# Kernel tuning notes

Measured on AMD Instinct MI355X. Metric: run time of the kernel, lower is better.

## Reference

```python
import jax, jax.numpy as jnp
import numpy as np
from jax import lax

TAU = 0.5       # opt.tau
EPSILON = 1e-3  # opt.epsilon


def setup_inputs() -> dict:
    key = jax.random.key(0)
    k1, k2, k3, k4 = jax.random.split(key, 4)
    B, Cin, H, W = 32, 64, 64, 64
    Cout, KS = 256, 5
    x = jax.random.normal(k1, (B, Cin, H, W), dtype=jnp.float32)
    # W_ff: OIHW conv kernel (Kaiming-ish scale)
    W_ff = jax.random.normal(k2, (Cout, Cin, KS, KS), dtype=jnp.float32) * (1.0 / np.sqrt(Cin * KS * KS))
    # W_rec: 1x1 recurrent conv, stored as [out, out]; small so the LCA loop converges
    W_rec = jax.random.normal(k3, (Cout, Cout), dtype=jnp.float32) * 0.01
    threshold = 0.1 * jax.random.normal(k4, (Cout,), dtype=jnp.float32)
    return {"x": x, "W_ff": W_ff, "W_rec": W_rec, "threshold": threshold, "max_n_iter": 20}


def _fro(v):
    return jnp.linalg.norm(v.ravel())


def _forward(x, W_ff, W_rec, threshold, max_n_iter):
    max_iter = max_n_iter * int(1.0 / TAU)
    # u_0 = W_ff * input  (valid conv, no bias)  -> [B, Cout, Ho, Wo]
    u0 = lax.conv_general_dilated(x, W_ff, window_strides=(1, 1), padding='VALID',
                                  dimension_numbers=('NCHW', 'OIHW', 'NCHW'))
    thr = threshold[None, :, None, None]
    a0 = jax.nn.relu(u0 - thr)
    u_init = jnp.zeros_like(u0)

    def cond(state):
        _, _, i, converged = state
        return jnp.logical_and(jnp.logical_not(converged), i <= max_iter)

    def body(state):
        u, a, i, _ = state
        # 1x1 recurrent conv == channel matmul
        rec = jnp.einsum('oi,bixy->boxy', W_rec, a)
        u_new = (1.0 - TAU) * u + TAU * (u0 - rec)
        a_new = jax.nn.relu(u_new - thr)
        converged = (_fro(u_new - u) / _fro(u_new)) < EPSILON
        return (u_new, a_new, i + 1, converged)

    _, a_final, _, _ = lax.while_loop(cond, body, (u_init, a0, jnp.int32(0), jnp.array(False)))
    # original torch code detaches activities throughout the loop and at return
    return lax.stop_gradient(a_final)


def reference(x, W_ff, W_rec, threshold, max_n_iter):
    return _forward(x, W_ff, W_rec, threshold, max_n_iter)
```

## Files before the change

kernel.cpp:

```cpp
#include <hip/hip_runtime.h>


typedef __attribute__((ext_vector_type(8))) short short8;
typedef __attribute__((ext_vector_type(4))) float f32x4;

#define NTOT 115200
#define CHW  262144
#define HW2  4096
#define LDA  264
#define LDC  40

__device__ __forceinline__ unsigned short f2bf(float f) {
  unsigned int u = __float_as_uint(f);
  unsigned int r = u + 0x7FFFu + ((u >> 16) & 1u);
  return (unsigned short)(r >> 16);
}
__device__ __forceinline__ float bf2f(unsigned short h) {
  return __uint_as_float(((unsigned int)h) << 16);
}
__device__ __forceinline__ unsigned short f2h(float f) {
  _Float16 x = (_Float16)f;
  unsigned short r;
  __builtin_memcpy(&r, &x, 2);
  return r;
}
__device__ __forceinline__ float h2f(unsigned short h) {
  _Float16 x;
  __builtin_memcpy(&x, &h, 2);
  return (float)x;
}

__global__ void cast_weights(const float* __restrict__ wff_f,
                             const float* __restrict__ wrec_f,
                             unsigned short* __restrict__ wff,
                             unsigned short* __restrict__ wrec_sw) {
  int tid = blockIdx.x * 256 + threadIdx.x;
  if (tid < 409600) {
    int o = tid / 1600, k = tid % 1600;
    int kk = k >> 6, ci = k & 63;
    wff[tid] = f2bf(wff_f[o * 1600 + ci * 25 + kk]);
  } else if (tid < 409600 + 65536) {
    int i = tid - 409600;
    int o = i >> 8, ic = i & 255;
    wrec_sw[(((ic >> 3) << 8) + o) * 8 + (ic & 7)] = f2bf(wrec_f[i]);
  }
}

__global__ __launch_bounds__(256) void transpose_x(
    const float* __restrict__ x, unsigned short* __restrict__ xt) {
  int g = blockIdx.x * 256 + threadIdx.x;
  const float* src = x + (long)(g >> 12) * CHW + (g & 4095);
  unsigned short* dst = xt + (long)g * 64;
#pragma unroll
  for (int oct = 0; oct < 8; ++oct) {
    alignas(16) unsigned short tmp[8];
#pragma unroll
    for (int d = 0; d < 8; ++d)
      tmp[d] = f2bf(src[(oct * 8 + d) * HW2]);
    *(int4*)(dst + oct * 8) = *(const int4*)tmp;
  }
}

__global__ __launch_bounds__(256) void conv_kernel(
    const unsigned short* __restrict__ xt,
    const unsigned short* __restrict__ wff,
    unsigned short* __restrict__ u0_fl) {
  __shared__ short As[128 * LDC];
  __shared__ short Bs[128 * LDC];
  const int t = threadIdx.x;
  const int n0 = blockIdx.x * 128;
  const int oc0 = blockIdx.y * 128;
  const int lane = t & 63, w = t >> 6;
  const int q = lane >> 4, r = lane & 15;
  const int woc = w >> 1, wn = w & 1;
  const int qt = t & 3, mrow = t >> 2;

  int xbase[2];
#pragma unroll
  for (int p = 0; p < 2; ++p) {
    int n = n0 + p * 64 + mrow;
    int bb = n / 3600, rem = n - bb * 3600;
    int yy = rem / 60, xx = rem - yy * 60;
    xbase[p] = (bb * 4096 + yy * 64 + xx) * 64 + qt * 8;
  }

  f32x4 acc[4][4];
#pragma unroll
  for (int i = 0; i < 4; i++)
#pragma unroll
    for (int j = 0; j < 4; j++) acc[i][j] = (f32x4){0.f, 0.f, 0.f, 0.f};

  for (int c = 0; c < 50; ++c) {
    const int k0 = c * 32;
    const int kk = c >> 1;
    const int ky = kk / 5, kx = kk - ky * 5;
    const int choff = (ky * 64 + kx) * 64 + (c & 1) * 32;

    __syncthreads();
#pragma unroll
    for (int p = 0; p < 2; ++p) {
      int m = p * 64 + mrow;
      *(int4*)(&Bs[m * LDC + qt * 8]) =
          *(const int4*)(wff + (oc0 + m) * 1600 + k0 + qt * 8);
    }
#pragma unroll
    for (int p = 0; p < 2; ++p) {
      int m = p * 64 + mrow;
      *(int4*)(&As[m * LDC + qt * 8]) = *(const int4*)(xt + xbase[p] + choff);
    }
    __syncthreads();

    short8 xf[4], wf[4];
#pragma unroll
    for (int j = 0; j < 4; j++)
      xf[j] = *(const short8*)(&As[(wn * 64 + j * 16 + r) * LDC + q * 8]);
#pragma unroll
    for (int i = 0; i < 4; i++)
      wf[i] = *(const short8*)(&Bs[(woc * 64 + i * 16 + r) * LDC + q * 8]);
#pragma unroll
    for (int i = 0; i < 4; i++)
#pragma unroll
      for (int j = 0; j < 4; j++)
        acc[i][j] = __builtin_amdgcn_mfma_f32_16x16x32_bf16(wf[i], xf[j],
                                                            acc[i][j], 0, 0, 0);
  }

  const int tile = blockIdx.x * 2 + wn;
#pragma unroll
  for (int j = 0; j < 4; j++) {
#pragma unroll
    for (int p = 0; p < 2; p++) {
      const int w_fl = blockIdx.y * 4 + woc * 2 + p;
      alignas(16) unsigned short up[8];
#pragma unroll
      for (int d = 0; d < 4; ++d) up[d] = f2h(acc[2 * p][j][d]);
#pragma unroll
      for (int d = 0; d < 4; ++d) up[4 + d] = f2h(acc[2 * p + 1][j][d]);
      *(int4*)(&u0_fl[tile * 16384 + j * 4096 + (w_fl * 64 + q * 16 + r) * 8]) =
          *(const int4*)up;
    }
  }
}

__device__ __forceinline__ void gemm_acc8(const short* a_lds,
                                          const unsigned short* __restrict__
                                              wrec_sw,
                                          int w, int q, int r,
                                          f32x4 acc[2][4]) {
#pragma unroll
  for (int i = 0; i < 2; i++)
#pragma unroll
    for (int j = 0; j < 4; j++) acc[i][j] = (f32x4){0.f, 0.f, 0.f, 0.f};

#pragma unroll
  for (int c = 0; c < 8; ++c) {
    short8 afr[2], bfr[4];
#pragma unroll
    for (int i = 0; i < 2; i++)
      afr[i] = *(const short8*)(wrec_sw +
               (((c * 4 + q) << 8) + w * 32 + i * 16 + r) * 8);
#pragma unroll
    for (int j = 0; j < 4; j++)
      bfr[j] = *(const short8*)(&a_lds[(j * 16 + r) * LDA + c * 32 + q * 8]);
#pragma unroll
    for (int i = 0; i < 2; i++)
#pragma unroll
      for (int j = 0; j < 4; j++)
        acc[i][j] = __builtin_amdgcn_mfma_f32_16x16x32_bf16(afr[i], bfr[j],
                                                            acc[i][j], 0, 0, 0);
  }
}

template <int FIRST>
__global__ __launch_bounds__(512, 4) void iter_quad(
    const unsigned short* __restrict__ wrec_sw,
    const unsigned short* __restrict__ u0, const float* __restrict__ thr,
    const unsigned short* __restrict__ uin,
    unsigned short* __restrict__ o1, unsigned short* __restrict__ o2,
    unsigned short* __restrict__ o3, unsigned short* __restrict__ o4,
    float* __restrict__ norms, int* __restrict__ flag, int it1) {
  __shared__ short a_lds[64 * LDA];
  __shared__ float red[64];

  const int t = threadIdx.x;
  if (!FIRST) {
    if (*(volatile int*)flag) return;
    bool hit = false;
#pragma unroll
    for (int rr = 0; rr < 4; ++rr) {
      float d = 0.f, n = 0.f;
#pragma unroll
      for (int s = 0; s < 8; ++s) {
        d += norms[(it1 - 4 + rr) * 16 + s];
        n += norms[(it1 - 4 + rr) * 16 + 8 + s];
      }
      hit = hit || (d < 1e-6f * n);
    }
    if (hit) {
      if (t == 0) *flag = 1;
      return;
    }
  }

  const int lane = t & 63, w = t >> 6;
  const int q = lane >> 4, r = lane & 15;
  const unsigned base = blockIdx.x * 16384 + t * 8;

  float thc[2][4];
#pragma unroll
  for (int i = 0; i < 2; ++i) {
    float4 th = *(const float4*)(thr + w * 32 + i * 16 + q * 4);
    thc[i][0] = th.x; thc[i][1] = th.y; thc[i][2] = th.z; thc[i][3] = th.w;
  }

  int4 sv[4], u0c[4];
#pragma unroll
  for (int j = 0; j < 4; ++j) {
    u0c[j] = *(const int4*)(u0 + base + j * 4096);
    sv[j] = FIRST ? u0c[j] : *(const int4*)(uin + base + j * 4096);
  }

  float d2[4], n2[4];
#pragma unroll
  for (int p = 0; p < 4; ++p) { d2[p] = 0.f; n2[p] = 0.f; }

#define QPHASE(PH, OUT)                                                       \
  {                                                                           \
    _Pragma("unroll")                                                         \
    for (int j = 0; j < 4; ++j) {                                             \
      const unsigned short* hs = (const unsigned short*)&sv[j];               \
      _Pragma("unroll")                                                       \
      for (int i = 0; i < 2; ++i) {                                           \
        alignas(8) unsigned short ap[4];                                      \
        _Pragma("unroll")                                                     \
        for (int d = 0; d < 4; ++d) {                                         \
          float a = h2f(hs[i * 4 + d]) - thc[i][d];                           \
          ap[d] = f2bf(a > 0.f ? a : 0.f);                                    \
        }                                                                     \
        *(uint2*)(&a_lds[(j * 16 + r) * LDA + w * 32 + i * 16 + q * 4]) =     \
            *(const uint2*)ap;                                                \
      }                                                                       \
    }                                                                         \
    __syncthreads();                                                          \
    f32x4 acc[2][4];                                                          \
    gemm_acc8(a_lds, wrec_sw, w, q, r, acc);                                  \
    _Pragma("unroll")                                                         \
    for (int j = 0; j < 4; ++j) {                                             \
      const unsigned short* us = (const unsigned short*)&u0c[j];              \
      const unsigned short* hs = (const unsigned short*)&sv[j];               \
      alignas(16) unsigned short up[8];                                       \
      _Pragma("unroll")                                                       \
      for (int i = 0; i < 2; ++i)                                             \
        _Pragma("unroll")                                                     \
        for (int d = 0; d < 4; ++d) {                                         \
          float uo = (FIRST && (PH) == 1) ? 0.f : h2f(hs[i * 4 + d]);         \
          float un = 0.5f * uo + 0.5f * (h2f(us[i * 4 + d]) - acc[i][j][d]);  \
          float df = un - uo;                                                 \
          d2[(PH)-1] += df * df;                                              \
          n2[(PH)-1] += un * un;                                              \
          up[i * 4 + d] = f2h(un);                                            \
        }                                                                     \
      sv[j] = *(const int4*)up;                                               \
      *(int4*)((OUT) + base + j * 4096) = sv[j];                              \
    }                                                                         \
    __syncthreads();                                                          \
  }

  QPHASE(1, o1)
  QPHASE(2, o2)
  QPHASE(3, o3)
  QPHASE(4, o4)
#undef QPHASE

#pragma unroll
  for (int off = 32; off; off >>= 1)
#pragma unroll
    for (int p = 0; p < 4; ++p) {
      d2[p] += __shfl_down(d2[p], off, 64);
      n2[p] += __shfl_down(n2[p], off, 64);
    }
  if (lane == 0)
#pragma unroll
    for (int p = 0; p < 4; ++p) {
      red[p * 16 + w] = d2[p];
      red[p * 16 + 8 + w] = n2[p];
    }
  __syncthreads();
  if (t == 0) {
    const int slot = blockIdx.x & 7;
#pragma unroll
    for (int p = 0; p < 4; ++p) {
      float a0 = 0.f, a1 = 0.f;
#pragma unroll
      for (int s = 0; s < 8; ++s) {
        a0 += red[p * 16 + s];
        a1 += red[p * 16 + 8 + s];
      }
      atomicAdd(&norms[(it1 + p) * 16 + slot], a0);
      atomicAdd(&norms[(it1 + p) * 16 + 8 + slot], a1);
    }
  }
}

template <int FIRST>
__global__ __launch_bounds__(512, 4) void iter_pair(
    const unsigned short* __restrict__ wrec_sw,
    const unsigned short* __restrict__ u0, const float* __restrict__ thr,
    const unsigned short* __restrict__ uin,
    unsigned short* __restrict__ uA, unsigned short* __restrict__ uB,
    float* __restrict__ norms, int* __restrict__ flag, int itA) {
  __shared__ short a_lds[64 * LDA];
  __shared__ float red[32];

  const int t = threadIdx.x;
  if (!FIRST) {
    if (*(volatile int*)flag) return;
    float dA = 0.f, nA = 0.f, dB = 0.f, nB = 0.f;
#pragma unroll
    for (int s = 0; s < 8; ++s) {
      dA += norms[(itA - 2) * 16 + s];
      nA += norms[(itA - 2) * 16 + 8 + s];
      dB += norms[(itA - 1) * 16 + s];
      nB += norms[(itA - 1) * 16 + 8 + s];
    }
    if (dA < 1e-6f * nA || dB < 1e-6f * nB) {
      if (t == 0) *flag = 1;
      return;
    }
  }

  const int lane = t & 63, w = t >> 6;
  const int q = lane >> 4, r = lane & 15;
  const unsigned base = blockIdx.x * 16384 + t * 8;

  float thc[2][4];
#pragma unroll
  for (int i = 0; i < 2; ++i) {
    float4 th = *(const float4*)(thr + w * 32 + i * 16 + q * 4);
    thc[i][0] = th.x; thc[i][1] = th.y; thc[i][2] = th.z; thc[i][3] = th.w;
  }

  int4 sv[4], u0c[4];
#pragma unroll
  for (int j = 0; j < 4; ++j) {
    u0c[j] = *(const int4*)(u0 + base + j * 4096);
    sv[j] = FIRST ? u0c[j] : *(const int4*)(uin + base + j * 4096);
  }

#pragma unroll
  for (int j = 0; j < 4; ++j) {
    const unsigned short* hs = (const unsigned short*)&sv[j];
#pragma unroll
    for (int i = 0; i < 2; ++i) {
      alignas(8) unsigned short ap[4];
#pragma unroll
      for (int d = 0; d < 4; ++d) {
        float a = h2f(hs[i * 4 + d]) - thc[i][d];
        ap[d] = f2bf(a > 0.f ? a : 0.f);
      }
      *(uint2*)(&a_lds[(j * 16 + r) * LDA + w * 32 + i * 16 + q * 4]) =
          *(const uint2*)ap;
    }
  }
  __syncthreads();

  f32x4 acc[2][4];
  gemm_acc8(a_lds, wrec_sw, w, q, r, acc);

  float d2A = 0.f, n2A = 0.f;
#pragma unroll
  for (int j = 0; j < 4; ++j) {
    const unsigned short* us = (const unsigned short*)&u0c[j];
    const unsigned short* hs = (const unsigned short*)&sv[j];
    alignas(16) unsigned short up[8];
#pragma unroll
    for (int i = 0; i < 2; ++i)
#pragma unroll
      for (int d = 0; d < 4; ++d) {
        float uo = FIRST ? 0.f : h2f(hs[i * 4 + d]);
        float un = 0.5f * uo + 0.5f * (h2f(us[i * 4 + d]) - acc[i][j][d]);
        float df = un - uo;
        d2A += df * df;
        n2A += un * un;
        up[i * 4 + d] = f2h(un);
      }
    sv[j] = *(const int4*)up;
    *(int4*)(uA + base + j * 4096) = sv[j];
  }
  __syncthreads();

#pragma unroll
  for (int j = 0; j < 4; ++j) {
    const unsigned short* hs = (const unsigned short*)&sv[j];
#pragma unroll
    for (int i = 0; i < 2; ++i) {
      alignas(8) unsigned short ap[4];
#pragma unroll
      for (int d = 0; d < 4; ++d) {
        float a = h2f(hs[i * 4 + d]) - thc[i][d];
        ap[d] = f2bf(a > 0.f ? a : 0.f);
      }
      *(uint2*)(&a_lds[(j * 16 + r) * LDA + w * 32 + i * 16 + q * 4]) =
          *(const uint2*)ap;
    }
  }
  __syncthreads();

  gemm_acc8(a_lds, wrec_sw, w, q, r, acc);

  float d2B = 0.f, n2B = 0.f;
#pragma unroll
  for (int j = 0; j < 4; ++j) {
    const unsigned short* us = (const unsigned short*)&u0c[j];
    const unsigned short* hs = (const unsigned short*)&sv[j];
    alignas(16) unsigned short up[8];
#pragma unroll
    for (int i = 0; i < 2; ++i)
#pragma unroll
      for (int d = 0; d < 4; ++d) {
        float uo = h2f(hs[i * 4 + d]);
        float un = 0.5f * uo + 0.5f * (h2f(us[i * 4 + d]) - acc[i][j][d]);
        float df = un - uo;
        d2B += df * df;
        n2B += un * un;
        up[i * 4 + d] = f2h(un);
      }
    *(int4*)(uB + base + j * 4096) = *(const int4*)up;
  }

#pragma unroll
  for (int off = 32; off; off >>= 1) {
    d2A += __shfl_down(d2A, off, 64);
    n2A += __shfl_down(n2A, off, 64);
    d2B += __shfl_down(d2B, off, 64);
    n2B += __shfl_down(n2B, off, 64);
  }
  if (lane == 0) {
    red[w] = d2A; red[8 + w] = n2A; red[16 + w] = d2B; red[24 + w] = n2B;
  }
  __syncthreads();
  if (t == 0) {
    float a0 = 0.f, a1 = 0.f, a2 = 0.f, a3 = 0.f;
#pragma unroll
    for (int s = 0; s < 8; ++s) {
      a0 += red[s]; a1 += red[8 + s]; a2 += red[16 + s]; a3 += red[24 + s];
    }
    const int slot = blockIdx.x & 7;
    atomicAdd(&norms[itA * 16 + slot], a0);
    atomicAdd(&norms[itA * 16 + 8 + slot], a1);
    atomicAdd(&norms[(itA + 1) * 16 + slot], a2);
    atomicAdd(&norms[(itA + 1) * 16 + 8 + slot], a3);
  }
}

template <int FIRST, int ROWS>
__global__ __launch_bounds__(512, 4) void iter_one(
    const unsigned short* __restrict__ wrec_sw,
    const unsigned short* __restrict__ u0, const float* __restrict__ thr,
    const unsigned short* __restrict__ uin, unsigned short* __restrict__ uout,
    float* __restrict__ norms, int* __restrict__ flag, int it) {
  __shared__ short a_lds[64 * LDA];
  __shared__ float red[16];

  const int t = threadIdx.x;
  if (!FIRST) {
    if (*(volatile int*)flag) return;
    bool hit = false;
#pragma unroll
    for (int rr = 0; rr < ROWS; ++rr) {
      float d = 0.f, n = 0.f;
#pragma unroll
      for (int s = 0; s < 8; ++s) {
        d += norms[(it - ROWS + rr) * 16 + s];
        n += norms[(it - ROWS + rr) * 16 + 8 + s];
      }
      hit = hit || (d < 1e-6f * n);
    }
    if (hit) {
      if (t == 0) *flag = 1;
      return;
    }
  }

  const int lane = t & 63, w = t >> 6;
  const int q = lane >> 4, r = lane & 15;
  const unsigned base = blockIdx.x * 16384 + t * 8;

  float thc[2][4];
#pragma unroll
  for (int i = 0; i < 2; ++i) {
    float4 th = *(const float4*)(thr + w * 32 + i * 16 + q * 4);
    thc[i][0] = th.x; thc[i][1] = th.y; thc[i][2] = th.z; thc[i][3] = th.w;
  }

  int4 sv[4], u0c[4];
#pragma unroll
  for (int j = 0; j < 4; ++j) {
    u0c[j] = *(const int4*)(u0 + base + j * 4096);
    sv[j] = FIRST ? u0c[j] : *(const int4*)(uin + base + j * 4096);
  }

#pragma unroll
  for (int j = 0; j < 4; ++j) {
    const unsigned short* hs = (const unsigned short*)&sv[j];
#pragma unroll
    for (int i = 0; i < 2; ++i) {
      alignas(8) unsigned short ap[4];
#pragma unroll
      for (int d = 0; d < 4; ++d) {
        float a = h2f(hs[i * 4 + d]) - thc[i][d];
        ap[d] = f2bf(a > 0.f ? a : 0.f);
      }
      *(uint2*)(&a_lds[(j * 16 + r) * LDA + w * 32 + i * 16 + q * 4]) =
          *(const uint2*)ap;
    }
  }
  __syncthreads();

  f32x4 acc[2][4];
  gemm_acc8(a_lds, wrec_sw, w, q, r, acc);

  float d2 = 0.f, n2 = 0.f;
#pragma unroll
  for (int j = 0; j < 4; ++j) {
    const unsigned short* us = (const unsigned short*)&u0c[j];
    const unsigned short* hs = (const unsigned short*)&sv[j];
    alignas(16) unsigned short up[8];
#pragma unroll
    for (int i = 0; i < 2; ++i)
#pragma unroll
      for (int d = 0; d < 4; ++d) {
        float uo = FIRST ? 0.f : h2f(hs[i * 4 + d]);
        float un = 0.5f * uo + 0.5f * (h2f(us[i * 4 + d]) - acc[i][j][d]);
        float df = un - uo;
        d2 += df * df;
        n2 += un * un;
        up[i * 4 + d] = f2h(un);
      }
    *(int4*)(uout + base + j * 4096) = *(const int4*)up;
  }

#pragma unroll
  for (int off = 32; off; off >>= 1) {
    d2 += __shfl_down(d2, off, 64);
    n2 += __shfl_down(n2, off, 64);
  }
  if (lane == 0) { red[w] = d2; red[8 + w] = n2; }
  __syncthreads();
  if (t == 0) {
    float a0 = 0.f, a1 = 0.f;
#pragma unroll
    for (int s = 0; s < 8; ++s) { a0 += red[s]; a1 += red[8 + s]; }
    const int slot = blockIdx.x & 7;
    atomicAdd(&norms[it * 16 + slot], a0);
    atomicAdd(&norms[it * 16 + 8 + slot], a1);
  }
}

__global__ __launch_bounds__(512) void final_sel(
    const unsigned short* __restrict__ b0, const unsigned short* __restrict__ b1,
    const unsigned short* __restrict__ b2, const unsigned short* __restrict__ b3,
    const float* __restrict__ norms, const float* __restrict__ thr,
    float* __restrict__ out) {
  int it = 1;
  for (; it <= 41; ++it) {
    float d = 0.f, n = 0.f;
    for (int s = 0; s < 8; ++s) {
      d += norms[it * 16 + s];
      n += norms[it * 16 + 8 + s];
    }
    if (d < 1e-6f * n) break;
  }
  if (it > 41) it = 41;
  const int k = (it - 1) & 3;
  const unsigned short* u = (k & 2) ? ((k & 1) ? b3 : b2)
                                    : ((k & 1) ? b1 : b0);

  const int t = threadIdx.x;
  const int lane = t & 63, w = t >> 6;
  const int q = lane >> 4, r = lane & 15;
  const unsigned base = blockIdx.x * 16384 + t * 8;

  float thc[2][4];
#pragma unroll
  for (int i = 0; i < 2; ++i) {
    float4 th = *(const float4*)(thr + w * 32 + i * 16 + q * 4);
    thc[i][0] = th.x; thc[i][1] = th.y; thc[i][2] = th.z; thc[i][3] = th.w;
  }

#pragma unroll
  for (int j = 0; j < 4; ++j) {
    int4 raw = *(const int4*)(u + base + j * 4096);
    const unsigned short* rs = (const unsigned short*)&raw;
    const int n = blockIdx.x * 64 + j * 16 + r;
    const int b = n / 3600, s = n - b * 3600;
    float* ob = out + (long)b * 921600 + s;
#pragma unroll
    for (int i = 0; i < 2; ++i)
#pragma unroll
      for (int d = 0; d < 4; ++d) {
        const int oc = w * 32 + i * 16 + q * 4 + d;
        float v = h2f(rs[i * 4 + d]) - thc[i][d];
        ob[oc * 3600] = v > 0.f ? v : 0.f;
      }
  }
}

extern "C" void kernel_launch(void* const* d_in, const int* in_sizes, int n_in,
                              void* d_out, int out_size, void* d_ws,
                              size_t ws_size, hipStream_t stream) {
  const float* x      = (const float*)d_in[0];
  const float* wff_f  = (const float*)d_in[1];
  const float* wrec_f = (const float*)d_in[2];
  const float* thr    = (const float*)d_in[3];
  float* out = (float*)d_out;

  char* ws = (char*)d_ws;
  int* flag = (int*)ws;
  float* norms = (float*)(ws + 64);
  unsigned short* wff     = (unsigned short*)(ws + 4096);
  unsigned short* wrec_sw = (unsigned short*)(ws + 823296);
  unsigned short* xt = (unsigned short*)(ws + 983040);
  unsigned short* uD = (unsigned short*)(ws + 983040);
  unsigned short* u0 = (unsigned short*)(ws + 59965440);
  unsigned short* uA = (unsigned short*)(ws + 118947840);
  unsigned short* uB = (unsigned short*)(ws + 177930240);
  unsigned short* uC = (unsigned short*)(ws + 236912640);
  const size_t NEED_QUAD = 236912640ULL + 58982400ULL;
  const size_t NEED_PAIR = 118947840ULL + 58982400ULL;

  hipMemsetAsync(d_ws, 0, 4096, stream);
  cast_weights<<<1856, 256, 0, stream>>>(wff_f, wrec_f, wff, wrec_sw);
  transpose_x<<<512, 256, 0, stream>>>(x, xt);
  conv_kernel<<<dim3(900, 2), 256, 0, stream>>>(xt, wff, u0);

  if (ws_size >= NEED_QUAD) {
    iter_quad<1><<<1800, 512, 0, stream>>>(wrec_sw, u0, thr, uD, uA, uB, uC,
                                           uD, norms, flag, 1);
    for (int it1 = 5; it1 <= 37; it1 += 4)
      iter_quad<0><<<1800, 512, 0, stream>>>(wrec_sw, u0, thr, uD, uA, uB, uC,
                                             uD, norms, flag, it1);
    iter_one<0, 4><<<1800, 512, 0, stream>>>(wrec_sw, u0, thr, uD, uA, norms,
                                             flag, 41);
    final_sel<<<1800, 512, 0, stream>>>(uA, uB, uC, uD, norms, thr, out);
  } else if (ws_size >= NEED_PAIR) {
    iter_pair<1><<<1800, 512, 0, stream>>>(wrec_sw, u0, thr, uD, uA, uD,
                                           norms, flag, 1);
    for (int itA = 3; itA <= 39; itA += 2)
      iter_pair<0><<<1800, 512, 0, stream>>>(wrec_sw, u0, thr, uD, uA, uD,
                                             norms, flag, itA);
    iter_one<0, 2><<<1800, 512, 0, stream>>>(wrec_sw, u0, thr, uD, uA, norms,
                                             flag, 41);
    final_sel<<<1800, 512, 0, stream>>>(uA, uD, uA, uD, norms, thr, out);
  } else {
    iter_one<1, 0><<<1800, 512, 0, stream>>>(wrec_sw, u0, thr, uD, uD, norms,
                                             flag, 1);
    for (int it = 2; it <= 41; ++it)
      iter_one<0, 2><<<1800, 512, 0, stream>>>(wrec_sw, u0, thr, uD, uD,
                                               norms, flag, it);
    final_sel<<<1800, 512, 0, stream>>>(uD, uD, uD, uD, norms, thr, out);
  }
}
```

Baseline: 991.1 us.

## Switch from four-iteration to three-iteration fused launches to cut workspace footprint

Replaces the kernel that fuses four LCA iterations per launch with one that fuses three, rotating among three state buffers instead of four. The total workspace need drops, and the final selection kernel is templated on the buffer rotation modulus. The plain __syncthreads in each phase becomes an explicit LDS-only wait plus s_barrier, which avoids waiting on outstanding global stores. The cost is more launches and more convergence-check points per run, plus an extra single-iteration tail launch.

```diff
diff --git a/kernel.cpp b/kernel.cpp
--- a/kernel.cpp
+++ b/kernel.cpp
@@ -9,6 +9,12 @@
 #define HW2  4096
 #define LDA  264
 #define LDC  40
+
+#define BAR_LDS()                                          \
+  do {                                                     \
+    asm volatile("s_waitcnt lgkmcnt(0)" ::: "memory");     \
+    __builtin_amdgcn_s_barrier();                          \
+  } while (0)
 
 __device__ __forceinline__ unsigned short f2bf(float f) {
   unsigned int u = __float_as_uint(f);
@@ -172,27 +178,27 @@
 }
 
 template <int FIRST>
-__global__ __launch_bounds__(512, 4) void iter_quad(
+__global__ __launch_bounds__(512, 4) void iter_tri(
     const unsigned short* __restrict__ wrec_sw,
     const unsigned short* __restrict__ u0, const float* __restrict__ thr,
     const unsigned short* __restrict__ uin,
     unsigned short* __restrict__ o1, unsigned short* __restrict__ o2,
-    unsigned short* __restrict__ o3, unsigned short* __restrict__ o4,
+    unsigned short* __restrict__ o3,
     float* __restrict__ norms, int* __restrict__ flag, int it1) {
   __shared__ short a_lds[64 * LDA];
-  __shared__ float red[64];
+  __shared__ float red[48];
 
   const int t = threadIdx.x;
   if (!FIRST) {
     if (*(volatile int*)flag) return;
     bool hit = false;
 #pragma unroll
-    for (int rr = 0; rr < 4; ++rr) {
+    for (int rr = 0; rr < 3; ++rr) {
       float d = 0.f, n = 0.f;
 #pragma unroll
       for (int s = 0; s < 8; ++s) {
-        d += norms[(it1 - 4 + rr) * 16 + s];
-        n += norms[(it1 - 4 + rr) * 16 + 8 + s];
+        d += norms[(it1 - 3 + rr) * 16 + s];
+        n += norms[(it1 - 3 + rr) * 16 + 8 + s];
       }
       hit = hit || (d < 1e-6f * n);
     }
@@ -220,9 +226,9 @@
     sv[j] = FIRST ? u0c[j] : *(const int4*)(uin + base + j * 4096);
   }
 
-  float d2[4], n2[4];
-#pragma unroll
-  for (int p = 0; p < 4; ++p) { d2[p] = 0.f; n2[p] = 0.f; }
+  float d2[3], n2[3];
+#pragma unroll
+  for (int p = 0; p < 3; ++p) { d2[p] = 0.f; n2[p] = 0.f; }
 
 #define QPHASE(PH, OUT)                                                       \
   {                                                                           \
@@ -241,7 +247,7 @@
             *(const uint2*)ap;                                                \
       }                                                                       \
     }                                                                         \
-    __syncthreads();                                                          \
+    BAR_LDS();                                                                \
     f32x4 acc[2][4];                                                          \
     gemm_acc8(a_lds, wrec_sw, w, q, r, acc);                                  \
     _Pragma("unroll")                                                         \
@@ -263,25 +269,24 @@
       sv[j] = *(const int4*)up;                                               \
       *(int4*)((OUT) + base + j * 4096) = sv[j];                              \
     }                                                                         \
-    __syncthreads();                                                          \
+    BAR_LDS();                                                                \
   }
 
   QPHASE(1, o1)
   QPHASE(2, o2)
   QPHASE(3, o3)
-  QPHASE(4, o4)
 #undef QPHASE
 
 #pragma unroll
   for (int off = 32; off; off >>= 1)
 #pragma unroll
-    for (int p = 0; p < 4; ++p) {
+    for (int p = 0; p < 3; ++p) {
       d2[p] += __shfl_down(d2[p], off, 64);
       n2[p] += __shfl_down(n2[p], off, 64);
     }
   if (lane == 0)
 #pragma unroll
-    for (int p = 0; p < 4; ++p) {
+    for (int p = 0; p < 3; ++p) {
       red[p * 16 + w] = d2[p];
       red[p * 16 + 8 + w] = n2[p];
     }
@@ -289,7 +294,7 @@
   if (t == 0) {
     const int slot = blockIdx.x & 7;
 #pragma unroll
-    for (int p = 0; p < 4; ++p) {
+    for (int p = 0; p < 3; ++p) {
       float a0 = 0.f, a1 = 0.f;
 #pragma unroll
       for (int s = 0; s < 8; ++s) {
@@ -557,9 +562,10 @@
   }
 }
 
+template <int MOD>
 __global__ __launch_bounds__(512) void final_sel(
     const unsigned short* __restrict__ b0, const unsigned short* __restrict__ b1,
-    const unsigned short* __restrict__ b2, const unsigned short* __restrict__ b3,
+    const unsigned short* __restrict__ b2,
     const float* __restrict__ norms, const float* __restrict__ thr,
     float* __restrict__ out) {
   int it = 1;
@@ -572,9 +578,8 @@
     if (d < 1e-6f * n) break;
   }
   if (it > 41) it = 41;
-  const int k = (it - 1) & 3;
-  const unsigned short* u = (k & 2) ? ((k & 1) ? b3 : b2)
-                                    : ((k & 1) ? b1 : b0);
+  const int k = (it - 1) % MOD;
+  const unsigned short* u = (k == 0) ? b0 : ((k == 1) ? b1 : b2);
 
   const int t = threadIdx.x;
   const int lane = t & 63, w = t >> 6;
@@ -621,12 +626,11 @@
   unsigned short* wff     = (unsigned short*)(ws + 4096);
   unsigned short* wrec_sw = (unsigned short*)(ws + 823296);
   unsigned short* xt = (unsigned short*)(ws + 983040);
-  unsigned short* uD = (unsigned short*)(ws + 983040);
+  unsigned short* s1 = (unsigned short*)(ws + 983040);
   unsigned short* u0 = (unsigned short*)(ws + 59965440);
-  unsigned short* uA = (unsigned short*)(ws + 118947840);
-  unsigned short* uB = (unsigned short*)(ws + 177930240);
-  unsigned short* uC = (unsigned short*)(ws + 236912640);
-  const size_t NEED_QUAD = 236912640ULL + 58982400ULL;
+  unsigned short* s2 = (unsigned short*)(ws + 118947840);
+  unsigned short* s3 = (unsigned short*)(ws + 177930240);
+  const size_t NEED_TRI  = 177930240ULL + 58982400ULL;
   const size_t NEED_PAIR = 118947840ULL + 58982400ULL;
 
   hipMemsetAsync(d_ws, 0, 4096, stream);
@@ -634,30 +638,32 @@
   transpose_x<<<512, 256, 0, stream>>>(x, xt);
   conv_kernel<<<dim3(900, 2), 256, 0, stream>>>(xt, wff, u0);
 
-  if (ws_size >= NEED_QUAD) {
-    iter_quad<1><<<1800, 512, 0, stream>>>(wrec_sw, u0, thr, uD, uA, uB, uC,
-                                           uD, norms, flag, 1);
-    for (int it1 = 5; it1 <= 37; it1 += 4)
-      iter_quad<0><<<1800, 512, 0, stream>>>(wrec_sw, u0, thr, uD, uA, uB, uC,
-                                             uD, norms, flag, it1);
-    iter_one<0, 4><<<1800, 512, 0, stream>>>(wrec_sw, u0, thr, uD, uA, norms,
+  if (ws_size >= NEED_TRI) {
+    iter_tri<1><<<1800, 512, 0, stream>>>(wrec_sw, u0, thr, s3, s1, s2, s3,
+                                          norms, flag, 1);
+    for (int it1 = 4; it1 <= 37; it1 += 3)
+      iter_tri<0><<<1800, 512, 0, stream>>>(wrec_sw, u0, thr, s3, s1, s2, s3,
+                                            norms, flag, it1);
+    iter_one<0, 3><<<1800, 512, 0, stream>>>(wrec_sw, u0, thr, s3, s1, norms,
+                                             flag, 40);
+    iter_one<0, 1><<<1800, 512, 0, stream>>>(wrec_sw, u0, thr, s1, s2, norms,
                                              flag, 41);
-    final_sel<<<1800, 512, 0, stream>>>(uA, uB, uC, uD, norms, thr, out);
+    final_sel<3><<<1800, 512, 0, stream>>>(s1, s2, s3, norms, thr, out);
   } else if (ws_size >= NEED_PAIR) {
-    iter_pair<1><<<1800, 512, 0, stream>>>(wrec_sw, u0, thr, uD, uA, uD,
+    iter_pair<1><<<1800, 512, 0, stream>>>(wrec_sw, u0, thr, s2, s1, s2,
                                            norms, flag, 1);
     for (int itA = 3; itA <= 39; itA += 2)
-      iter_pair<0><<<1800, 512, 0, stream>>>(wrec_sw, u0, thr, uD, uA, uD,
+      iter_pair<0><<<1800, 512, 0, stream>>>(wrec_sw, u0, thr, s2, s1, s2,
                                              norms, flag, itA);
-    iter_one<0, 2><<<1800, 512, 0, stream>>>(wrec_sw, u0, thr, uD, uA, norms,
+    iter_one<0, 2><<<1800, 512, 0, stream>>>(wrec_sw, u0, thr, s2, s1, norms,
                                              flag, 41);
-    final_sel<<<1800, 512, 0, stream>>>(uA, uD, uA, uD, norms, thr, out);
+    final_sel<2><<<1800, 512, 0, stream>>>(s1, s2, s2, norms, thr, out);
   } else {
-    iter_one<1, 0><<<1800, 512, 0, stream>>>(wrec_sw, u0, thr, uD, uD, norms,
+    iter_one<1, 0><<<1800, 512, 0, stream>>>(wrec_sw, u0, thr, s1, s1, norms,
                                              flag, 1);
     for (int it = 2; it <= 41; ++it)
-      iter_one<0, 2><<<1800, 512, 0, stream>>>(wrec_sw, u0, thr, uD, uD,
+      iter_one<0, 1><<<1800, 512, 0, stream>>>(wrec_sw, u0, thr, s1, s1,
                                                norms, flag, it);
-    final_sel<<<1800, 512, 0, stream>>>(uD, uD, uD, uD, norms, thr, out);
-  }
-}
+    final_sel<1><<<1800, 512, 0, stream>>>(s1, s1, s1, norms, thr, out);
+  }
+}
```

Result: slower. 1.243 ms (+25.5%).
